# Kernel optimization log

Hardware: AMD Instinct MI355X
Metric: run time of the kernel (lower is better)

Reference implementation:

```python
import jax, jax.numpy as jnp
import numpy as np

N, E, B = 50000, 800000, 64
D_IN, D_E = 192, 64
NUM_OUT = 256


def setup_inputs() -> dict:
    key = jax.random.key(0)
    ks = jax.random.split(key, 30)
    rn = lambda k, s: jax.random.normal(k, s, dtype=jnp.float32) * 0.05
    return {
        "x": jax.random.normal(ks[0], (N, D_IN), jnp.float32),
        "edge_index": jax.random.randint(ks[1], (2, E), 0, N, dtype=jnp.int32),
        "edge_attr": jax.random.normal(ks[2], (E, D_E), jnp.float32),
        "batch": jnp.sort(jax.random.randint(ks[3], (N,), 0, B, dtype=jnp.int32)),
        "W1": rn(ks[4], (D_IN, 256)), "as1": rn(ks[5], (4, 64)), "ad1": rn(ks[6], (4, 64)),
        "We1": rn(ks[7], (D_E, 256)), "ae1": rn(ks[8], (4, 64)), "b1": rn(ks[9], (256,)),
        "W2": rn(ks[10], (256, 256)), "as2": rn(ks[11], (4, 64)), "ad2": rn(ks[12], (4, 64)),
        "We2": rn(ks[13], (D_E, 256)), "ae2": rn(ks[14], (4, 64)), "b2": rn(ks[15], (256,)),
        "W3": rn(ks[16], (256, 512)), "as3": rn(ks[17], (4, 128)), "ad3": rn(ks[18], (4, 128)),
        "We3": rn(ks[19], (D_E, 512)), "ae3": rn(ks[20], (4, 128)), "b3": rn(ks[21], (128,)),
        "Wa": rn(ks[22], (128, NUM_OUT)), "ba": rn(ks[23], (NUM_OUT,)),
        "Wv": rn(ks[24], (128, 1)), "bv": rn(ks[25], (1,)),
    }


def reference(x, edge_index, edge_attr, batch,
              W1, as1, ad1, We1, ae1, b1,
              W2, as2, ad2, We2, ae2, b2,
              W3, as3, ad3, We3, ae3, b3,
              Wa, ba, Wv, bv):
    Nn = x.shape[0]
    src0, dst0 = edge_index[0], edge_index[1]
    # PyG add_self_loops(fill_value='mean'): self-loop edge_attr = mean of incoming edge_attr
    deg = jax.ops.segment_sum(jnp.ones_like(dst0, dtype=x.dtype), dst0, num_segments=Nn)
    loop_attr = jax.ops.segment_sum(edge_attr, dst0, num_segments=Nn) / jnp.maximum(deg, 1.0)[:, None]
    loop = jnp.arange(Nn, dtype=src0.dtype)
    src = jnp.concatenate([src0, loop])
    dst = jnp.concatenate([dst0, loop])
    ea = jnp.concatenate([edge_attr, loop_attr], axis=0)

    def gat(h, W, a_s, a_d, We, a_e, bias, concat):
        Hh, C = a_s.shape
        hs = (h @ W).reshape(Nn, Hh, C)                       # [N,H,C]
        al_s = (hs * a_s).sum(-1)                             # [N,H]
        al_d = (hs * a_d).sum(-1)                             # [N,H]
        al_e = ((ea @ We).reshape(-1, Hh, C) * a_e).sum(-1)   # [E+N,H]
        alpha = jax.nn.leaky_relu(al_s[src] + al_d[dst] + al_e, 0.2)
        amax = jax.ops.segment_max(alpha, dst, num_segments=Nn)
        w = jnp.exp(alpha - amax[dst])
        denom = jax.ops.segment_sum(w, dst, num_segments=Nn)
        w = w / (denom[dst] + 1e-16)                          # scatter-softmax over dst
        out = jax.ops.segment_sum(hs[src] * w[..., None], dst, num_segments=Nn)
        out = out.reshape(Nn, Hh * C) if concat else out.mean(axis=1)
        return out + bias

    h = jax.nn.relu(gat(x, W1, as1, ad1, We1, ae1, b1, True))
    h = jax.nn.relu(gat(h, W2, as2, ad2, We2, ae2, b2, True))
    h = gat(h, W3, as3, ad3, We3, ae3, b3, False)
    cnt = jax.ops.segment_sum(jnp.ones((Nn,), h.dtype), batch, num_segments=B)
    g = jax.ops.segment_sum(h, batch, num_segments=B) / jnp.maximum(cnt, 1.0)[:, None]
    logits = g @ Wa + ba
    value = g @ Wv + bv
    return jnp.concatenate([logits, value], axis=-1)  # [B, num_outputs+1]
```

## Files before the change

### kernel.cpp

```cpp
#include <hip/hip_runtime.h>
#include <hip/hip_bf16.h>


typedef __attribute__((ext_vector_type(8))) short short8;
typedef __attribute__((ext_vector_type(4))) float floatx4;
typedef __attribute__((ext_vector_type(4))) unsigned int uintx4;

#define DEV __device__ __forceinline__

DEV unsigned short f2b(float f) {
  union { float f; unsigned u; } v; v.f = f;
  unsigned r = v.u + 0x7FFFu + ((v.u >> 16) & 1u);
  return (unsigned short)(r >> 16);
}
DEV float b2f(unsigned short u) {
  union { unsigned u; float f; } v; v.u = ((unsigned)u) << 16;
  return v.f;
}

__global__ void k_deg(const int* __restrict__ dst, int* __restrict__ deg, int E) {
  int e = blockIdx.x * 256 + threadIdx.x;
  if (e < E) atomicAdd(&deg[dst[e]], 1);
}

__global__ __launch_bounds__(256) void k_scan1(const int* __restrict__ deg,
    int* __restrict__ rowptr, int* __restrict__ bsum, int N) {
  __shared__ int sd[256];
  int b = blockIdx.x, tid = threadIdx.x;
  int i0 = b * 1024 + tid * 4;
  int v[4]; int s = 0;
#pragma unroll
  for (int j = 0; j < 4; j++) { int i = i0 + j; v[j] = (i < N) ? deg[i] : 0; s += v[j]; }
  sd[tid] = s;
  __syncthreads();
  for (int off = 1; off < 256; off <<= 1) {
    int t = (tid >= off) ? sd[tid - off] : 0;
    __syncthreads();
    sd[tid] += t;
    __syncthreads();
  }
  int run = sd[tid] - s;
#pragma unroll
  for (int j = 0; j < 4; j++) { int i = i0 + j; if (i < N) rowptr[i] = run; run += v[j]; }
  if (tid == 255) bsum[b] = sd[255];
}

__global__ __launch_bounds__(256) void k_scan2(int* __restrict__ bsum, int nb) {
  __shared__ int sd[256];
  int tid = threadIdx.x;
  int v = (tid < nb) ? bsum[tid] : 0;
  sd[tid] = v;
  __syncthreads();
  for (int off = 1; off < 256; off <<= 1) {
    int t = (tid >= off) ? sd[tid - off] : 0;
    __syncthreads();
    sd[tid] += t;
    __syncthreads();
  }
  if (tid < nb) bsum[tid] = sd[tid] - v;
}

__global__ __launch_bounds__(256) void k_scan3(int* __restrict__ rowptr,
    int* __restrict__ cursor, const int* __restrict__ bsum, int N, int E) {
  int b = blockIdx.x, tid = threadIdx.x;
  int add = bsum[b];
  int i0 = b * 1024 + tid * 4;
#pragma unroll
  for (int j = 0; j < 4; j++) {
    int i = i0 + j;
    if (i < N) { int r = rowptr[i] + add; rowptr[i] = r; cursor[i] = r; }
  }
  if (b == 0 && tid == 0) rowptr[N] = E;
}

__global__ void k_scatter(const int* __restrict__ src, const int* __restrict__ dst,
    int* __restrict__ cursor, int2* __restrict__ csr, int E) {
  int e = blockIdx.x * 256 + threadIdx.x;
  if (e < E) {
    int d = dst[e];
    int pos = atomicAdd(&cursor[d], 1);
    csr[pos] = make_int2(src[e], e);
  }
}

__global__ void k_wt(const float* __restrict__ W, unsigned short* __restrict__ Wt,
                     int K, int Nout) {
  int idx = blockIdx.x * 256 + threadIdx.x;
  if (idx < K * Nout) {
    int n = idx / K, k = idx - n * K;
    Wt[idx] = f2b(W[(size_t)k * Nout + n]);
  }
}

__global__ void k_wep(const float* __restrict__ We1, const float* __restrict__ ae1,
                      const float* __restrict__ We2, const float* __restrict__ ae2,
                      const float* __restrict__ We3, const float* __restrict__ ae3,
                      unsigned short* __restrict__ Wept) {
  int t = blockIdx.x * 256 + threadIdx.x;
  int j = t >> 6, c = t & 63;
  int L = j >> 2, h = j & 3;
  const float* We = (L == 0) ? We1 : (L == 1) ? We2 : We3;
  const float* ae = (L == 0) ? ae1 : (L == 1) ? ae2 : ae3;
  int C = (L == 2) ? 128 : 64;
  int HC = 4 * C;
  float s = 0.f;
  for (int cc = 0; cc < C; cc++) s += We[(size_t)c * HC + h * C + cc] * ae[h * C + cc];
  Wept[j * 64 + c] = f2b(s);
  if (t < 256) {
    int jj = 12 + (t >> 6);
    Wept[jj * 64 + (t & 63)] = 0;
  }
}

template<bool A_F32, int OUT_MODE, bool DO_ALD>
__global__ __launch_bounds__(256) void k_gemm(const void* __restrict__ Ap,
    const unsigned short* __restrict__ Bt, void* __restrict__ Cp,
    int M, int Nout, int K, int EN,
    const float* __restrict__ a_s, const float* __restrict__ a_d,
    float* __restrict__ als, float* __restrict__ ald) {
  __shared__ unsigned short As[64][40];
  __shared__ unsigned short Bs[64][40];
  const int tid = threadIdx.x;
  const int wave = tid >> 6, lane = tid & 63;
  const int quad = lane >> 4, l16 = lane & 15;
  const int m0 = blockIdx.x * 64, n0 = blockIdx.y * 64;
  const int arow = tid >> 2, acg = (tid & 3) * 8;
  floatx4 acc[4] = {{0,0,0,0},{0,0,0,0},{0,0,0,0},{0,0,0,0}};
  for (int k0 = 0; k0 < K; k0 += 32) {
    {
      int gm = m0 + arow;
      unsigned short tmp[8];
      if (A_F32) {
        const float* Af = (const float*)Ap;
        if (gm < M) {
          const float4* p = (const float4*)(Af + (size_t)gm * K + k0 + acg);
          float4 u0 = p[0], u1 = p[1];
          tmp[0]=f2b(u0.x); tmp[1]=f2b(u0.y); tmp[2]=f2b(u0.z); tmp[3]=f2b(u0.w);
          tmp[4]=f2b(u1.x); tmp[5]=f2b(u1.y); tmp[6]=f2b(u1.z); tmp[7]=f2b(u1.w);
        } else {
#pragma unroll
          for (int j = 0; j < 8; j++) tmp[j] = 0;
        }
      } else {
        const unsigned short* Ab = (const unsigned short*)Ap;
        uint4 u = {0,0,0,0};
        if (gm < M) u = *(const uint4*)(Ab + (size_t)gm * K + k0 + acg);
        *(uint4*)tmp = u;
      }
      *(uint4*)&As[arow][acg] = *(uint4*)tmp;
      int gn = n0 + arow;
      uint4 bv = {0,0,0,0};
      if (gn < Nout) bv = *(const uint4*)(Bt + (size_t)gn * K + k0 + acg);
      *(uint4*)&Bs[arow][acg] = bv;
    }
    __syncthreads();
    short8 a = *(const short8*)&As[wave * 16 + l16][quad * 8];
#pragma unroll
    for (int t = 0; t < 4; t++) {
      short8 b = *(const short8*)&Bs[t * 16 + l16][quad * 8];
      acc[t] = __builtin_amdgcn_mfma_f32_16x16x32_bf16(a, b, acc[t], 0, 0, 0);
    }
    __syncthreads();
  }
#pragma unroll
  for (int t = 0; t < 4; t++) {
#pragma unroll
    for (int r = 0; r < 4; r++) {
      int row = m0 + wave * 16 + quad * 4 + r;
      int col = n0 + t * 16 + l16;
      float v = acc[t][r];
      if (OUT_MODE == 0) {
        if (row < M && col < Nout)
          ((unsigned short*)Cp)[(size_t)row * Nout + col] = f2b(v);
      } else {
        if (row < M && col < 12)
          ((float*)Cp)[((size_t)(col >> 2) * EN + row) * 4 + (col & 3)] = v;
      }
    }
  }
  if constexpr (DO_ALD) {
    int h = (n0 * 4) / Nout;
#pragma unroll
    for (int r = 0; r < 4; r++) {
      float ps = 0.f, pd = 0.f;
#pragma unroll
      for (int t = 0; t < 4; t++) {
        int col = n0 + t * 16 + l16;
        float v = acc[t][r];
        ps += v * a_s[col];
        pd += v * a_d[col];
      }
#pragma unroll
      for (int off = 1; off < 16; off <<= 1) {
        ps += __shfl_xor(ps, off, 64);
        pd += __shfl_xor(pd, off, 64);
      }
      int row = m0 + wave * 16 + quad * 4 + r;
      if (l16 == 0 && row < M) {
        atomicAdd(&als[row * 4 + h], ps);
        atomicAdd(&ald[row * 4 + h], pd);
      }
    }
  }
}

__global__ void k_loop_ale(const int* __restrict__ rowptr, const int2* __restrict__ csr,
                           float* __restrict__ ale, int N, int E) {
  int n = blockIdx.x * 256 + threadIdx.x;
  if (n >= N) return;
  const size_t EN = (size_t)E + N;
  int s = rowptr[n], e = rowptr[n + 1];
  float a[12];
#pragma unroll
  for (int j = 0; j < 12; j++) a[j] = 0.f;
  for (int p = s; p < e; p++) {
    int eid = csr[p].y;
#pragma unroll
    for (int L = 0; L < 3; L++) {
      float4 v = *(const float4*)(ale + (L * EN + eid) * 4);
      a[L * 4 + 0] += v.x; a[L * 4 + 1] += v.y;
      a[L * 4 + 2] += v.z; a[L * 4 + 3] += v.w;
    }
  }
  float inv = 1.0f / (float)((e - s) > 1 ? (e - s) : 1);
#pragma unroll
  for (int L = 0; L < 3; L++)
    *(float4*)(ale + (L * EN + E + n) * 4) =
        make_float4(a[L*4+0]*inv, a[L*4+1]*inv, a[L*4+2]*inv, a[L*4+3]*inv);
}

template<int LPN, int MODE>
__global__ __launch_bounds__(256) void k_agg(const unsigned short* __restrict__ hs,
    const int* __restrict__ rowptr, const int2* __restrict__ csr,
    const float* __restrict__ ale,
    const float* __restrict__ als, const float* __restrict__ ald,
    const float* __restrict__ bias, unsigned short* __restrict__ outb,
    float* __restrict__ outf, int N, int E) {
  const int FPL = 32;
  const int HC  = LPN * FPL;
  const int NG  = 64 / LPN;
  __shared__ float s_w[4][NG][LPN][4];
  __shared__ int   s_s[4][NG][LPN];
  const int wave = threadIdx.x >> 6;
  const int lane = threadIdx.x & 63;
  const int grp  = lane / LPN;
  const int sl   = lane % LPN;
  const int hd   = sl >> (LPN >> 3);
  const int node = blockIdx.x * (4 * NG) + wave * NG + grp;
  if (node >= N) return;
  int start = rowptr[node];
  int cnt   = rowptr[node + 1] - start;
  int total = cnt + 1;
  const float4 aldv   = *(const float4*)(ald + (size_t)node * 4);
  const float4 selfev = *(const float4*)(ale + ((size_t)E + node) * 4);
  const float4 selfsv = *(const float4*)(als + (size_t)node * 4);
  int    psidx = node;
  float4 pev = selfev, psv = selfsv;
  if (sl < cnt) {
    int2 se = csr[start + sl];
    psidx = se.x;
    pev = *(const float4*)(ale + (size_t)se.y * 4);
    psv = *(const float4*)(als + (size_t)se.x * 4);
  }
  float m0=-1e30f, m1=-1e30f, m2=-1e30f, m3=-1e30f;
  float d0=0.f, d1=0.f, d2=0.f, d3=0.f;
  float acc[FPL];
#pragma unroll
  for (int j = 0; j < FPL; j++) acc[j] = 0.f;
  for (int base = 0; base < total; base += LPN) {
    int ei = base + sl;
    bool active = ei < total;
    float a0=-1e30f, a1=-1e30f, a2=-1e30f, a3=-1e30f;
    int sidx = psidx;
    if (active) {
      a0 = psv.x + aldv.x + pev.x;
      a1 = psv.y + aldv.y + pev.y;
      a2 = psv.z + aldv.z + pev.z;
      a3 = psv.w + aldv.w + pev.w;
      a0 = a0 > 0.f ? a0 : 0.2f * a0;
      a1 = a1 > 0.f ? a1 : 0.2f * a1;
      a2 = a2 > 0.f ? a2 : 0.2f * a2;
      a3 = a3 > 0.f ? a3 : 0.2f * a3;
    }
    float c0=a0, c1=a1, c2=a2, c3=a3;
#pragma unroll
    for (int off = LPN / 2; off > 0; off >>= 1) {
      c0 = fmaxf(c0, __shfl_xor(c0, off, 64));
      c1 = fmaxf(c1, __shfl_xor(c1, off, 64));
      c2 = fmaxf(c2, __shfl_xor(c2, off, 64));
      c3 = fmaxf(c3, __shfl_xor(c3, off, 64));
    }
    float n0v = fmaxf(m0, c0), n1v = fmaxf(m1, c1), n2v = fmaxf(m2, c2), n3v = fmaxf(m3, c3);
    float p0 = active ? __expf(a0 - n0v) : 0.f;
    float p1 = active ? __expf(a1 - n1v) : 0.f;
    float p2 = active ? __expf(a2 - n2v) : 0.f;
    float p3 = active ? __expf(a3 - n3v) : 0.f;
    float s0=p0, s1=p1, s2=p2, s3=p3;
#pragma unroll
    for (int off = LPN / 2; off > 0; off >>= 1) {
      s0 += __shfl_xor(s0, off, 64);
      s1 += __shfl_xor(s1, off, 64);
      s2 += __shfl_xor(s2, off, 64);
      s3 += __shfl_xor(s3, off, 64);
    }
    float r0 = __expf(m0 - n0v), r1 = __expf(m1 - n1v);
    float r2 = __expf(m2 - n2v), r3 = __expf(m3 - n3v);
    d0 = d0 * r0 + s0; d1 = d1 * r1 + s1; d2 = d2 * r2 + s2; d3 = d3 * r3 + s3;
    float rh = hd == 0 ? r0 : hd == 1 ? r1 : hd == 2 ? r2 : r3;
#pragma unroll
    for (int j = 0; j < FPL; j++) acc[j] *= rh;
    m0 = n0v; m1 = n1v; m2 = n2v; m3 = n3v;
    *(float4*)&s_w[wave][grp][sl][0] = make_float4(p0, p1, p2, p3);
    s_s[wave][grp][sl] = sidx;
    __threadfence_block();
    if (base + LPN < total) {
      int nei = base + LPN + sl;
      psidx = node; pev = selfev; psv = selfsv;
      if (nei < cnt) {
        int2 se = csr[start + nei];
        psidx = se.x;
        pev = *(const float4*)(ale + (size_t)se.y * 4);
        psv = *(const float4*)(als + (size_t)se.x * 4);
      }
    }
    int chunk = total - base; if (chunk > LPN) chunk = LPN;
    int t = 0;
    for (; t + 2 <= chunk; t += 2) {
      float w0 = s_w[wave][grp][t][hd];
      float w1 = s_w[wave][grp][t + 1][hd];
      int   q0 = s_s[wave][grp][t];
      int   q1 = s_s[wave][grp][t + 1];
      const uintx4* p0p = (const uintx4*)(hs + (size_t)q0 * HC + sl * FPL);
      const uintx4* p1p = (const uintx4*)(hs + (size_t)q1 * HC + sl * FPL);
      uintx4 v0[4], v1[4];
#pragma unroll
      for (int q = 0; q < 4; q++) v0[q] = p0p[q];
#pragma unroll
      for (int q = 0; q < 4; q++) v1[q] = p1p[q];
      asm volatile("" :: "v"(v0[0]), "v"(v0[1]), "v"(v0[2]), "v"(v0[3]),
                         "v"(v1[0]), "v"(v1[1]), "v"(v1[2]), "v"(v1[3]));
#pragma unroll
      for (int q = 0; q < 4; q++) {
        uintx4 x = v0[q];
#pragma unroll
        for (int k = 0; k < 4; k++) {
          float lo = __uint_as_float(x[k] << 16);
          float hi = __uint_as_float(x[k] & 0xffff0000u);
          acc[q * 8 + k * 2 + 0] += w0 * lo;
          acc[q * 8 + k * 2 + 1] += w0 * hi;
        }
      }
#pragma unroll
      for (int q = 0; q < 4; q++) {
        uintx4 x = v1[q];
#pragma unroll
        for (int k = 0; k < 4; k++) {
          float lo = __uint_as_float(x[k] << 16);
          float hi = __uint_as_float(x[k] & 0xffff0000u);
          acc[q * 8 + k * 2 + 0] += w1 * lo;
          acc[q * 8 + k * 2 + 1] += w1 * hi;
        }
      }
    }
    if (t < chunk) {
      float w0 = s_w[wave][grp][t][hd];
      int   q0 = s_s[wave][grp][t];
      const uintx4* p0p = (const uintx4*)(hs + (size_t)q0 * HC + sl * FPL);
      uintx4 v0[4];
#pragma unroll
      for (int q = 0; q < 4; q++) v0[q] = p0p[q];
#pragma unroll
      for (int q = 0; q < 4; q++) {
        uintx4 x = v0[q];
#pragma unroll
        for (int k = 0; k < 4; k++) {
          float lo = __uint_as_float(x[k] << 16);
          float hi = __uint_as_float(x[k] & 0xffff0000u);
          acc[q * 8 + k * 2 + 0] += w0 * lo;
          acc[q * 8 + k * 2 + 1] += w0 * hi;
        }
      }
    }
  }
  float dh = hd == 0 ? d0 : hd == 1 ? d1 : hd == 2 ? d2 : d3;
  float inv = 1.0f / (dh + 1e-16f);
  if constexpr (MODE == 0) {
    unsigned short tmp[FPL];
#pragma unroll
    for (int j = 0; j < FPL; j++) {
      float v = acc[j] * inv + bias[sl * FPL + j];
      tmp[j] = f2b(fmaxf(v, 0.f));
    }
    unsigned short* op = outb + (size_t)node * HC + sl * FPL;
#pragma unroll
    for (int q = 0; q < 4; q++) ((uint4*)op)[q] = ((uint4*)tmp)[q];
  } else {
#pragma unroll
    for (int j = 0; j < FPL; j++) {
      float v = acc[j] * inv;
      v += __shfl_xor(v, 4, 64);
      v += __shfl_xor(v, 8, 64);
      acc[j] = v * 0.25f;
    }
    if (sl < 4) {
      float* op = outf + (size_t)node * (4 * FPL) + sl * FPL;
#pragma unroll
      for (int j = 0; j < FPL; j++) op[j] = acc[j] + bias[sl * FPL + j];
    }
  }
}

__global__ __launch_bounds__(256) void k_pool(const float* __restrict__ out3,
    const int* __restrict__ bat, float* __restrict__ g, int* __restrict__ cntb, int N) {
  int wid = blockIdx.x * 4 + (threadIdx.x >> 6);
  int lane = threadIdx.x & 63;
  int per = (N + 255) / 256;
  int s = wid * per, e = s + per;
  if (e > N) e = N;
  if (s >= e) return;
  int cur = bat[s];
  float ax = 0.f, ay = 0.f; int run = 0;
  for (int n = s; n < e; n++) {
    int b = bat[n];
    if (b != cur) {
      atomicAdd(&g[cur * 128 + lane * 2], ax);
      atomicAdd(&g[cur * 128 + lane * 2 + 1], ay);
      if (lane == 0) atomicAdd(&cntb[cur], run);
      ax = 0.f; ay = 0.f; run = 0; cur = b;
    }
    float2 v = *(const float2*)(out3 + (size_t)n * 128 + lane * 2);
    ax += v.x; ay += v.y; run++;
  }
  atomicAdd(&g[cur * 128 + lane * 2], ax);
  atomicAdd(&g[cur * 128 + lane * 2 + 1], ay);
  if (lane == 0) atomicAdd(&cntb[cur], run);
}

__global__ __launch_bounds__(320) void k_final(const float* __restrict__ g,
    const int* __restrict__ cntb, const float* __restrict__ Wa, const float* __restrict__ ba,
    const float* __restrict__ Wv, const float* __restrict__ bv, float* __restrict__ out) {
  __shared__ float gm[128];
  int b = blockIdx.x, t = threadIdx.x;
  if (t < 128) {
    float c = (float)cntb[b];
    gm[t] = g[b * 128 + t] / fmaxf(c, 1.f);
  }
  __syncthreads();
  if (t < 257) {
    float acc = 0.f;
    if (t < 256) {
      for (int k = 0; k < 128; k++) acc += gm[k] * Wa[k * 256 + t];
      acc += ba[t];
    } else {
      for (int k = 0; k < 128; k++) acc += gm[k] * Wv[k];
      acc += bv[0];
    }
    out[b * 257 + t] = acc;
  }
}

extern "C" void kernel_launch(void* const* d_in, const int* in_sizes, int n_in,
                              void* d_out, int out_size, void* d_ws, size_t ws_size,
                              hipStream_t stream) {
  const float* x   = (const float*)d_in[0];
  const int*   ei  = (const int*)  d_in[1];
  const float* ea  = (const float*)d_in[2];
  const int*   bat = (const int*)  d_in[3];
  const float* W1  = (const float*)d_in[4];
  const float* as1 = (const float*)d_in[5];
  const float* ad1 = (const float*)d_in[6];
  const float* We1 = (const float*)d_in[7];
  const float* ae1 = (const float*)d_in[8];
  const float* b1  = (const float*)d_in[9];
  const float* W2  = (const float*)d_in[10];
  const float* as2 = (const float*)d_in[11];
  const float* ad2 = (const float*)d_in[12];
  const float* We2 = (const float*)d_in[13];
  const float* ae2 = (const float*)d_in[14];
  const float* b2  = (const float*)d_in[15];
  const float* W3  = (const float*)d_in[16];
  const float* as3 = (const float*)d_in[17];
  const float* ad3 = (const float*)d_in[18];
  const float* We3 = (const float*)d_in[19];
  const float* ae3 = (const float*)d_in[20];
  const float* b3  = (const float*)d_in[21];
  const float* Wa  = (const float*)d_in[22];
  const float* ba  = (const float*)d_in[23];
  const float* Wv  = (const float*)d_in[24];
  const float* bv  = (const float*)d_in[25];
  (void)n_in; (void)out_size; (void)ws_size;

  const int N = in_sizes[0] / 192;
  const int E = in_sizes[1] / 2;
  const size_t EN = (size_t)E + N;
  const int* srcv = ei;
  const int* dstv = ei + E;
  const int nb = (N + 1023) / 1024;

  size_t off = 0;
  auto alloc = [&](size_t bytes) -> char* {
    char* p = (char*)d_ws + off;
    off += (bytes + 255) & ~(size_t)255;
    return p;
  };
  int* deg     = (int*)alloc((size_t)N * 4);
  int* rowptr  = (int*)alloc((size_t)(N + 1) * 4);
  int* cursor  = (int*)alloc((size_t)N * 4);
  int* bsum    = (int*)alloc(256 * 4);
  int2* csr    = (int2*)alloc((size_t)E * 8);
  float* ale   = (float*)alloc(3 * EN * 4 * 4);
  unsigned short* Wept = (unsigned short*)alloc(16 * 64 * 2);
  unsigned short* W1t  = (unsigned short*)alloc(256 * 192 * 2);
  unsigned short* W2t  = (unsigned short*)alloc(256 * 256 * 2);
  unsigned short* W3t  = (unsigned short*)alloc(512 * 256 * 2);
  unsigned short* hs   = (unsigned short*)alloc((size_t)N * 512 * 2);
  unsigned short* h1   = (unsigned short*)alloc((size_t)N * 256 * 2);
  unsigned short* h2   = (unsigned short*)alloc((size_t)N * 256 * 2);
  float* out3  = (float*)alloc((size_t)N * 128 * 4);
  float* als_all = (float*)alloc((size_t)N * 4 * 4 * 6);
  float* g     = (float*)alloc(64 * 128 * 4 + 64 * 4);
  int* cntb    = (int*)(g + 64 * 128);
  float* als1 = als_all + (size_t)N * 4 * 0;
  float* ald1 = als_all + (size_t)N * 4 * 1;
  float* als2 = als_all + (size_t)N * 4 * 2;
  float* ald2 = als_all + (size_t)N * 4 * 3;
  float* als3 = als_all + (size_t)N * 4 * 4;
  float* ald3 = als_all + (size_t)N * 4 * 5;

  hipMemsetAsync(deg, 0, (size_t)N * 4, stream);
  hipMemsetAsync(als_all, 0, (size_t)N * 4 * 4 * 6, stream);
  hipMemsetAsync(g, 0, 64 * 128 * 4 + 64 * 4, stream);

  k_deg<<<(E + 255) / 256, 256, 0, stream>>>(dstv, deg, E);
  k_scan1<<<nb, 256, 0, stream>>>(deg, rowptr, bsum, N);
  k_scan2<<<1, 256, 0, stream>>>(bsum, nb);
  k_scan3<<<nb, 256, 0, stream>>>(rowptr, cursor, bsum, N, E);
  k_scatter<<<(E + 255) / 256, 256, 0, stream>>>(srcv, dstv, cursor, csr, E);
  k_wt<<<(192 * 256 + 255) / 256, 256, 0, stream>>>(W1, W1t, 192, 256);
  k_wt<<<(256 * 256 + 255) / 256, 256, 0, stream>>>(W2, W2t, 256, 256);
  k_wt<<<(256 * 512 + 255) / 256, 256, 0, stream>>>(W3, W3t, 256, 512);
  k_wep<<<3, 256, 0, stream>>>(We1, ae1, We2, ae2, We3, ae3, Wept);
  k_gemm<true, 2, false><<<dim3((E + 63) / 64, 1), 256, 0, stream>>>(
      ea, Wept, ale, E, 16, 64, (int)EN, nullptr, nullptr, nullptr, nullptr);
  k_loop_ale<<<(N + 255) / 256, 256, 0, stream>>>(rowptr, csr, ale, N, E);
  k_gemm<true, 0, true><<<dim3((N + 63) / 64, 4), 256, 0, stream>>>(
      x, W1t, hs, N, 256, 192, 0, as1, ad1, als1, ald1);
  k_agg<8, 0><<<(N + 31) / 32, 256, 0, stream>>>(
      hs, rowptr, csr, ale + 0 * EN * 4, als1, ald1, b1, h1, nullptr, N, E);
  k_gemm<false, 0, true><<<dim3((N + 63) / 64, 4), 256, 0, stream>>>(
      h1, W2t, hs, N, 256, 256, 0, as2, ad2, als2, ald2);
  k_agg<8, 0><<<(N + 31) / 32, 256, 0, stream>>>(
      hs, rowptr, csr, ale + 1 * EN * 4, als2, ald2, b2, h2, nullptr, N, E);
  k_gemm<false, 0, true><<<dim3((N + 63) / 64, 8), 256, 0, stream>>>(
      h2, W3t, hs, N, 512, 256, 0, as3, ad3, als3, ald3);
  k_agg<16, 1><<<(N + 15) / 16, 256, 0, stream>>>(
      hs, rowptr, csr, ale + 2 * EN * 4, als3, ald3, b3, nullptr, out3, N, E);
  k_pool<<<64, 256, 0, stream>>>(out3, bat, g, cntb, N);
  k_final<<<64, 320, 0, stream>>>(g, cntb, Wa, ba, Wv, bv, (float*)d_out);
}
```

Before: 1.068 ms.

## Bucket CSR neighbors by source-index range to improve gather locality

Builds the CSR with each destination row split into 8 sub-buckets keyed by the high bits of the source index (src>>13), so neighbors within a row come out roughly sorted by source. The aggregation kernels then gather hs rows in a more ordered address pattern, which is meant to improve cache locality of the random source-feature gathers. It costs an 8x larger degree/scan array and a larger scan, and assumes N fits in 8 buckets of 8192 (N<=65536).

```diff
diff --git a/kernel.cpp b/kernel.cpp
--- a/kernel.cpp
+++ b/kernel.cpp
@@ -18,9 +18,10 @@
   return v.f;
 }
 
-__global__ void k_deg(const int* __restrict__ dst, int* __restrict__ deg, int E) {
+__global__ void k_deg2(const int* __restrict__ src, const int* __restrict__ dst,
+                       int* __restrict__ deg2, int E) {
   int e = blockIdx.x * 256 + threadIdx.x;
-  if (e < E) atomicAdd(&deg[dst[e]], 1);
+  if (e < E) atomicAdd(&deg2[(size_t)dst[e] * 8 + (src[e] >> 13)], 1);
 }
 
 __global__ __launch_bounds__(256) void k_scan1(const int* __restrict__ deg,
@@ -45,13 +46,13 @@
   if (tid == 255) bsum[b] = sd[255];
 }
 
-__global__ __launch_bounds__(256) void k_scan2(int* __restrict__ bsum, int nb) {
-  __shared__ int sd[256];
+__global__ __launch_bounds__(512) void k_scan2(int* __restrict__ bsum, int nb) {
+  __shared__ int sd[512];
   int tid = threadIdx.x;
   int v = (tid < nb) ? bsum[tid] : 0;
   sd[tid] = v;
   __syncthreads();
-  for (int off = 1; off < 256; off <<= 1) {
+  for (int off = 1; off < 512; off <<= 1) {
     int t = (tid >= off) ? sd[tid - off] : 0;
     __syncthreads();
     sd[tid] += t;
@@ -77,9 +78,9 @@
     int* __restrict__ cursor, int2* __restrict__ csr, int E) {
   int e = blockIdx.x * 256 + threadIdx.x;
   if (e < E) {
-    int d = dst[e];
-    int pos = atomicAdd(&cursor[d], 1);
-    csr[pos] = make_int2(src[e], e);
+    int s = src[e], d = dst[e];
+    int pos = atomicAdd(&cursor[(size_t)d * 8 + (s >> 13)], 1);
+    csr[pos] = make_int2(s, e);
   }
 }
 
@@ -204,12 +205,12 @@
   }
 }
 
-__global__ void k_loop_ale(const int* __restrict__ rowptr, const int2* __restrict__ csr,
+__global__ void k_loop_ale(const int* __restrict__ rowptr2, const int2* __restrict__ csr,
                            float* __restrict__ ale, int N, int E) {
   int n = blockIdx.x * 256 + threadIdx.x;
   if (n >= N) return;
   const size_t EN = (size_t)E + N;
-  int s = rowptr[n], e = rowptr[n + 1];
+  int s = rowptr2[(size_t)n * 8], e = rowptr2[(size_t)n * 8 + 8];
   float a[12];
 #pragma unroll
   for (int j = 0; j < 12; j++) a[j] = 0.f;
@@ -231,7 +232,7 @@
 
 template<int LPN, int MODE>
 __global__ __launch_bounds__(256) void k_agg(const unsigned short* __restrict__ hs,
-    const int* __restrict__ rowptr, const int2* __restrict__ csr,
+    const int* __restrict__ rowptr2, const int2* __restrict__ csr,
     const float* __restrict__ ale,
     const float* __restrict__ als, const float* __restrict__ ald,
     const float* __restrict__ bias, unsigned short* __restrict__ outb,
@@ -248,8 +249,8 @@
   const int hd   = sl >> (LPN >> 3);
   const int node = blockIdx.x * (4 * NG) + wave * NG + grp;
   if (node >= N) return;
-  int start = rowptr[node];
-  int cnt   = rowptr[node + 1] - start;
+  int start = rowptr2[(size_t)node * 8];
+  int cnt   = rowptr2[(size_t)node * 8 + 8] - start;
   int total = cnt + 1;
   const float4 aldv   = *(const float4*)(ald + (size_t)node * 4);
   const float4 selfev = *(const float4*)(ale + ((size_t)E + node) * 4);
@@ -495,7 +496,8 @@
   const size_t EN = (size_t)E + N;
   const int* srcv = ei;
   const int* dstv = ei + E;
-  const int nb = (N + 1023) / 1024;
+  const int N2 = N * 8;
+  const int nbB = (N2 + 1023) / 1024;
 
   size_t off = 0;
   auto alloc = [&](size_t bytes) -> char* {
@@ -503,10 +505,10 @@
     off += (bytes + 255) & ~(size_t)255;
     return p;
   };
-  int* deg     = (int*)alloc((size_t)N * 4);
-  int* rowptr  = (int*)alloc((size_t)(N + 1) * 4);
-  int* cursor  = (int*)alloc((size_t)N * 4);
-  int* bsum    = (int*)alloc(256 * 4);
+  int* deg2    = (int*)alloc((size_t)N2 * 4);
+  int* rowptr2 = (int*)alloc((size_t)(N2 + 1) * 4);
+  int* cursor2 = (int*)alloc((size_t)N2 * 4);
+  int* bsum    = (int*)alloc(512 * 4);
   int2* csr    = (int2*)alloc((size_t)E * 8);
   float* ale   = (float*)alloc(3 * EN * 4 * 4);
   unsigned short* Wept = (unsigned short*)alloc(16 * 64 * 2);
@@ -527,34 +529,34 @@
   float* als3 = als_all + (size_t)N * 4 * 4;
   float* ald3 = als_all + (size_t)N * 4 * 5;
 
-  hipMemsetAsync(deg, 0, (size_t)N * 4, stream);
+  hipMemsetAsync(deg2, 0, (size_t)N2 * 4, stream);
   hipMemsetAsync(als_all, 0, (size_t)N * 4 * 4 * 6, stream);
   hipMemsetAsync(g, 0, 64 * 128 * 4 + 64 * 4, stream);
 
-  k_deg<<<(E + 255) / 256, 256, 0, stream>>>(dstv, deg, E);
-  k_scan1<<<nb, 256, 0, stream>>>(deg, rowptr, bsum, N);
-  k_scan2<<<1, 256, 0, stream>>>(bsum, nb);
-  k_scan3<<<nb, 256, 0, stream>>>(rowptr, cursor, bsum, N, E);
-  k_scatter<<<(E + 255) / 256, 256, 0, stream>>>(srcv, dstv, cursor, csr, E);
+  k_deg2<<<(E + 255) / 256, 256, 0, stream>>>(srcv, dstv, deg2, E);
+  k_scan1<<<nbB, 256, 0, stream>>>(deg2, rowptr2, bsum, N2);
+  k_scan2<<<1, 512, 0, stream>>>(bsum, nbB);
+  k_scan3<<<nbB, 256, 0, stream>>>(rowptr2, cursor2, bsum, N2, E);
+  k_scatter<<<(E + 255) / 256, 256, 0, stream>>>(srcv, dstv, cursor2, csr, E);
   k_wt<<<(192 * 256 + 255) / 256, 256, 0, stream>>>(W1, W1t, 192, 256);
   k_wt<<<(256 * 256 + 255) / 256, 256, 0, stream>>>(W2, W2t, 256, 256);
   k_wt<<<(256 * 512 + 255) / 256, 256, 0, stream>>>(W3, W3t, 256, 512);
   k_wep<<<3, 256, 0, stream>>>(We1, ae1, We2, ae2, We3, ae3, Wept);
   k_gemm<true, 2, false><<<dim3((E + 63) / 64, 1), 256, 0, stream>>>(
       ea, Wept, ale, E, 16, 64, (int)EN, nullptr, nullptr, nullptr, nullptr);
-  k_loop_ale<<<(N + 255) / 256, 256, 0, stream>>>(rowptr, csr, ale, N, E);
+  k_loop_ale<<<(N + 255) / 256, 256, 0, stream>>>(rowptr2, csr, ale, N, E);
   k_gemm<true, 0, true><<<dim3((N + 63) / 64, 4), 256, 0, stream>>>(
       x, W1t, hs, N, 256, 192, 0, as1, ad1, als1, ald1);
   k_agg<8, 0><<<(N + 31) / 32, 256, 0, stream>>>(
-      hs, rowptr, csr, ale + 0 * EN * 4, als1, ald1, b1, h1, nullptr, N, E);
+      hs, rowptr2, csr, ale + 0 * EN * 4, als1, ald1, b1, h1, nullptr, N, E);
   k_gemm<false, 0, true><<<dim3((N + 63) / 64, 4), 256, 0, stream>>>(
       h1, W2t, hs, N, 256, 256, 0, as2, ad2, als2, ald2);
   k_agg<8, 0><<<(N + 31) / 32, 256, 0, stream>>>(
-      hs, rowptr, csr, ale + 1 * EN * 4, als2, ald2, b2, h2, nullptr, N, E);
+      hs, rowptr2, csr, ale + 1 * EN * 4, als2, ald2, b2, h2, nullptr, N, E);
   k_gemm<false, 0, true><<<dim3((N + 63) / 64, 8), 256, 0, stream>>>(
       h2, W3t, hs, N, 512, 256, 0, as3, ad3, als3, ald3);
   k_agg<16, 1><<<(N + 15) / 16, 256, 0, stream>>>(
-      hs, rowptr, csr, ale + 2 * EN * 4, als3, ald3, b3, nullptr, out3, N, E);
+      hs, rowptr2, csr, ale + 2 * EN * 4, als3, ald3, b3, nullptr, out3, N, E);
   k_pool<<<64, 256, 0, stream>>>(out3, bat, g, cntb, N);
   k_final<<<64, 320, 0, stream>>>(g, cntb, Wa, ba, Wv, bv, (float*)d_out);
 }
```

Measured after the change: 1.068 ms. About the same (-0.0%).
